# Optimization experiments

Hardware: AMD Instinct MI355X
Metric: run time of the kernel (lower is better)

Reference implementation:

```python
import jax, jax.numpy as jnp
import numpy as np

NEG_SLOPE = 0.1   # LeakyReLU slope
EPS = 1e-5        # GroupNorm eps
GROUPS = 8        # out_feat // 16 = 128 // 16
NSAMPLE = 16      # naggre (k in KNN)
FEAT = 128        # feat_dim


def leaky(x):
    return jnp.where(x >= 0, x, NEG_SLOPE * x)


def gnorm(x, gamma, beta):
    # GroupNorm over channel dim 1; works for [B,C,N] and [B,C,N,K]
    B, C = x.shape[0], x.shape[1]
    sh = x.shape
    xg = x.reshape(B, GROUPS, -1)
    m = xg.mean(-1, keepdims=True)
    v = xg.var(-1, keepdims=True)
    xg = (xg - m) * jax.lax.rsqrt(v + EPS)
    br = (1, C) + (1,) * (len(sh) - 2)
    return xg.reshape(sh) * gamma.reshape(br) + beta.reshape(br)


def conv1(x, W, b):  # 1x1 Conv1d: x [B,C,N]
    return jnp.einsum('oc,bcn->bon', W, x) + b[None, :, None]


def conv2(x, W, b):  # 1x1 Conv2d: x [B,C,N,K]
    return jnp.einsum('oc,bcnk->bonk', W, x) + b[None, :, None, None]


def knn_idx(xyz, k):
    # xyz [B,3,N] -> idx [B,N,k] of k nearest points (self included)
    pts = xyz.transpose(0, 2, 1)                      # [B,N,3]
    sq = jnp.sum(pts * pts, axis=-1)                  # [B,N]
    d2 = sq[:, :, None] + sq[:, None, :] - 2.0 * jnp.einsum('bnc,bmc->bnm', pts, pts)
    _, idx = jax.lax.top_k(-d2, k)
    return idx


# grouping_operation: feat [B,C,N], idx [B,N,K] -> [B,C,N,K]
group = jax.vmap(lambda f, i: f[:, i])


def setup_inputs() -> dict:
    key = jax.random.key(0)
    ks = jax.random.split(key, 32)
    s = 0.05
    d = {
        'xyz': jax.random.normal(ks[0], (2, 3, 8192), jnp.float32),
        'feat': jax.random.normal(ks[1], (2, FEAT, 8192), jnp.float32),
        'W_pre': jax.random.normal(ks[2], (FEAT, FEAT), jnp.float32) * s,
        'b_pre': jnp.zeros((FEAT,), jnp.float32),
        'W_pos1': jax.random.normal(ks[3], (FEAT, 3), jnp.float32) * s,
        'b_pos1': jnp.zeros((FEAT,), jnp.float32),
        'g_pos1': jnp.ones((FEAT,), jnp.float32),
        'be_pos1': jnp.zeros((FEAT,), jnp.float32),
        'W_pos2': jax.random.normal(ks[4], (FEAT, FEAT), jnp.float32) * s,
        'b_pos2': jnp.zeros((FEAT,), jnp.float32),
        'W_q': jax.random.normal(ks[5], (FEAT, FEAT), jnp.float32) * s,
        'b_q': jnp.zeros((FEAT,), jnp.float32),
        'W_k': jax.random.normal(ks[6], (FEAT, FEAT), jnp.float32) * s,
        'b_k': jnp.zeros((FEAT,), jnp.float32),
        'W_v': jax.random.normal(ks[7], (FEAT, FEAT), jnp.float32) * s,
        'b_v': jnp.zeros((FEAT,), jnp.float32),
        'W_att1': jax.random.normal(ks[8], (FEAT, FEAT), jnp.float32) * s,
        'b_att1': jnp.zeros((FEAT,), jnp.float32),
        'g_att1': jnp.ones((FEAT,), jnp.float32),
        'be_att1': jnp.zeros((FEAT,), jnp.float32),
        'W_att2': jax.random.normal(ks[9], (FEAT, FEAT), jnp.float32) * s,
        'b_att2': jnp.zeros((FEAT,), jnp.float32),
        'W_post': jax.random.normal(ks[10], (FEAT, FEAT), jnp.float32) * s,
        'b_post': jnp.zeros((FEAT,), jnp.float32),
        'g_post': jnp.ones((FEAT,), jnp.float32),
        'be_post': jnp.zeros((FEAT,), jnp.float32),
    }
    return d


def reference(xyz, feat, W_pre, b_pre, W_pos1, b_pos1, g_pos1, be_pos1,
              W_pos2, b_pos2, W_q, b_q, W_k, b_k, W_v, b_v,
              W_att1, b_att1, g_att1, be_att1, W_att2, b_att2,
              W_post, b_post, g_post, be_post):
    idx = knn_idx(xyz, NSAMPLE)                       # [B,N,K]
    new_feat = conv1(feat, W_pre, b_pre)              # [B,C,N]
    rel = group(xyz, idx) - xyz[:, :, :, None]        # [B,3,N,K]
    pos = conv2(rel, W_pos1, b_pos1)
    pos = leaky(gnorm(pos, g_pos1, be_pos1))
    pos = conv2(pos, W_pos2, b_pos2)                  # [B,C,N,K]
    q = conv1(new_feat, W_q, b_q)
    k = group(conv1(new_feat, W_k, b_k), idx)
    v = group(conv1(new_feat, W_v, b_v), idx)
    att = q[:, :, :, None] - k + pos
    att = conv2(att, W_att1, b_att1)
    att = leaky(gnorm(att, g_att1, be_att1))
    att = conv2(att, W_att2, b_att2)
    att = jax.nn.softmax(att, axis=3)                 # softmax over neighbors
    out = jnp.sum(att * v, axis=3) + new_feat         # [B,C,N]
    out = leaky(gnorm(conv1(out, W_post, b_post), g_post, be_post))
    return out
```

## Files before the change

kernel.cpp:

```cpp
#include <hip/hip_runtime.h>
#include <hip/hip_bf16.h>
#include <float.h>

#define B_ 2
#define N_ 8192
#define C_ 128
#define K_ 16
#define G_ 8
#define NK_ (N_*K_)
#define BN_ (B_*N_)
#define BNK_ (B_*NK_)
#define CN_ (C_*N_)
#define NEG 0.1f
#define EPSV 1e-5f

#define GR_ 24
#define NC_ (GR_*GR_*GR_)
#define GLOF -6.0f
#define GHF 0.5f
#define KNN_MARGIN 2e-4f
#define EMPTY_KEY 0x7FEFFFFFFFFFFFFFull

typedef __attribute__((ext_vector_type(4))) float f32x4;
typedef __attribute__((ext_vector_type(8))) short s16x8;
typedef __attribute__((ext_vector_type(4))) short s16x4;

__device__ __forceinline__ float leakyf(float x){ return x >= 0.f ? x : NEG*x; }
__device__ __forceinline__ short f2b(float x){
  union { __hip_bfloat16 b; short s; } u; u.b = __float2bfloat16(x); return u.s;
}
__device__ __forceinline__ float b2f(short s){
  union { __hip_bfloat16 b; short s; } u; u.s = s; return __bfloat162float(u.b);
}

__device__ __forceinline__ int dpp_shr1_i(int x){
  return __builtin_amdgcn_update_dpp(x, x, 0x111, 0xF, 0xF, false);
}
__device__ __forceinline__ unsigned long long dpp_shr1_u64(unsigned long long x){
  union { unsigned long long q; int i[2]; } u; u.q = x;
  u.i[0] = dpp_shr1_i(u.i[0]);
  u.i[1] = dpp_shr1_i(u.i[1]);
  return u.q;
}
__device__ __forceinline__ unsigned long long readlane_u64(unsigned long long x, int l){
  union { unsigned long long q; int i[2]; } u; u.q = x;
  union { unsigned long long q; int i[2]; } r;
  r.i[0] = __builtin_amdgcn_readlane(u.i[0], l);
  r.i[1] = __builtin_amdgcn_readlane(u.i[1], l);
  return r.q;
}
__device__ __forceinline__ unsigned long long d2key(double d2, int idx){
  d2 = fmax(d2, 0.0);
  union { double d; unsigned long long q; } u; u.d = d2;
  return (u.q & ~0x1FFFull) | (unsigned long long)idx;
}
__device__ __forceinline__ double key_upper_d2(unsigned long long k){
  union { unsigned long long q; double d; } u; u.q = k | 0x1FFFull;
  return u.d;
}
__device__ __forceinline__ int cell1(float x){
  int c = (int)floorf((x - GLOF)*(1.0f/GHF));
  return min(max(c, 0), GR_-1);
}

template<int CTRL>
__device__ __forceinline__ float dppf(float x){
  union { float f; int i; } u; u.f = x;
  u.i = __builtin_amdgcn_update_dpp(0, u.i, CTRL, 0xF, 0xF, true);
  return u.f;
}
__device__ __forceinline__ float red16(float x){
  x += dppf<0xB1>(x);
  x += dppf<0x4E>(x);
  x += dppf<0x141>(x);
  x += dppf<0x140>(x);
  return x;
}

__global__ __launch_bounds__(256) void pack_featb_kernel(const float* __restrict__ xyz,
    const float* __restrict__ feat, float4* __restrict__ pt4, ushort* __restrict__ fb,
    int* __restrict__ cellCnt){
  int e = blockIdx.x*256 + threadIdx.x;
  int b = e >> 13, n = e & (N_-1);
  const float* xb = xyz + b*3*N_;
  float x = xb[n], y = xb[N_+n], z = xb[2*N_+n];
  pt4[e] = make_float4(x, y, z, x*x + y*y + z*z);
  atomicAdd(&cellCnt[b*NC_ + (cell1(z)*GR_ + cell1(y))*GR_ + cell1(x)], 1);
  const float* xin = feat + b*CN_ + n;
  #pragma unroll
  for (int c0 = 0; c0 < C_; c0 += 8){
    s16x8 o8;
    #pragma unroll
    for (int i = 0; i < 8; i++) o8[i] = f2b(xin[(size_t)(c0+i)*N_]);
    *(s16x8*)(fb + (size_t)e*C_ + c0) = o8;
  }
}

__global__ __launch_bounds__(1024) void scan_kernel(const int* __restrict__ cnt,
    int* __restrict__ cellStart, int* __restrict__ cellCur){
  __shared__ int bs[1024];
  int t = threadIdx.x;
  int base = t*27;
  int s = 0;
  for (int i = 0; i < 27; i++) s += cnt[base+i];
  bs[t] = s;
  __syncthreads();
  for (int off = 1; off < 1024; off <<= 1){
    int v = (t >= off) ? bs[t-off] : 0;
    __syncthreads();
    bs[t] += v;
    __syncthreads();
  }
  int run = (t == 0) ? 0 : bs[t-1];
  for (int i = 0; i < 27; i++){
    cellStart[base+i] = run;
    cellCur[base+i]  = run;
    run += cnt[base+i];
  }
  if (t == 1023) cellStart[2*NC_] = BN_;
}

__global__ __launch_bounds__(256) void scatter_kernel(const float4* __restrict__ pt4,
    int* __restrict__ cellCur, float4* __restrict__ spts, int* __restrict__ sidx){
  int e = blockIdx.x*256 + threadIdx.x;
  int b = e >> 13;
  float4 p = pt4[e];
  int cid = b*NC_ + (cell1(p.z)*GR_ + cell1(p.y))*GR_ + cell1(p.x);
  int slot = atomicAdd(&cellCur[cid], 1);
  spts[slot] = p;
  sidx[slot] = e & (N_-1);
}

__global__ __launch_bounds__(512) void knn_kernel(const float4* __restrict__ pt4,
    const float4* __restrict__ spts, const int* __restrict__ sidx,
    const int* __restrict__ cellStart, int* __restrict__ idxo){
  int lane = threadIdx.x & 63, wid = threadIdx.x >> 6;
  int qg = blockIdx.x*8 + wid;
  int b = qg >> 13;
  float4 qp = spts[qg];
  int nq = sidx[qg];
  double qx = qp.x, qy = qp.y, qz = qp.z;
  double qsq = qx*qx + qy*qy + qz*qz;
  float qx2 = -2.f*qp.x, qy2 = -2.f*qp.y, qz2 = -2.f*qp.z;
  unsigned long long mykey = EMPTY_KEY;
  float cmpv = FLT_MAX;
  int ci = cell1(qp.x), cj = cell1(qp.y), ck = cell1(qp.z);

  auto process = [&](unsigned long long m, unsigned long long keyv){
    while (m){
      int src = __ffsll(m) - 1; m &= m - 1;
      unsigned long long kn = readlane_u64(keyv, src);
      bool less = kn < mykey;
      unsigned long long bm = __ballot(less) & 0xFFFFull;
      if (bm){
        int pos = __ffsll(bm) - 1;
        unsigned long long pk = dpp_shr1_u64(mykey);
        if (lane < 16){
          if (lane > pos) mykey = pk;
          else if (lane == pos) mykey = kn;
        }
      }
    }
  };

  auto do_range = [&](int cid0, int cid1){
    int s = cellStart[cid0], e = cellStart[cid1+1];
    for (int off = s; off < e; off += 64){
      int t = off + lane;
      bool valid = t < e;
      float4 pp = make_float4(0.f, 0.f, 0.f, 3.0e38f);
      int oi = 0;
      if (valid){ pp = spts[t]; oi = sidx[t]; }
      float f = fmaf(pp.x, qx2, fmaf(pp.y, qy2, fmaf(pp.z, qz2, pp.w)));
      unsigned long long m = __ballot(valid && (f < cmpv));
      if (m){
        double px = pp.x, py = pp.y, pz = pp.z;
        double psq = px*px + py*py + pz*pz;
        double dot = qx*px + qy*py + qz*pz;
        process(m, d2key(qsq + psq - 2.0*dot, oi));
        cmpv = fminf(cmpv, (float)(key_upper_d2(readlane_u64(mykey, 15)) - qsq) + KNN_MARGIN);
      }
    }
  };

  int x0 = max(ci-1, 0), x1 = min(ci+1, GR_-1);
  int cbase = b*NC_;
  do_range(cbase + (ck*GR_ + cj)*GR_ + x0, cbase + (ck*GR_ + cj)*GR_ + x1);
  for (int dz = -1; dz <= 1; dz++){
    int z = ck + dz; if (z < 0 || z >= GR_) continue;
    for (int dy = -1; dy <= 1; dy++){
      int y = cj + dy; if (y < 0 || y >= GR_) continue;
      if ((dy | dz) == 0) continue;
      do_range(cbase + (z*GR_ + y)*GR_ + x0, cbase + (z*GR_ + y)*GR_ + x1);
    }
  }

  double thr_up = key_upper_d2(readlane_u64(mykey, 15));
  if (thr_up > (double)GHF*(double)GHF){
    mykey = EMPTY_KEY;
    const float4* pts = pt4 + (b << 13);
    for (int t0 = 0; t0 < N_; t0 += 64){
      float4 pp = pts[t0 + lane];
      float f = fmaf(pp.x, qx2, fmaf(pp.y, qy2, fmaf(pp.z, qz2, pp.w)));
      unsigned long long m = __ballot(f < cmpv);
      if (m){
        double px = pp.x, py = pp.y, pz = pp.z;
        double psq = px*px + py*py + pz*pz;
        double dot = qx*px + qy*py + qz*pz;
        process(m, d2key(qsq + psq - 2.0*dot, t0 + lane));
        cmpv = fminf(cmpv, (float)(key_upper_d2(readlane_u64(mykey, 15)) - qsq) + KNN_MARGIN);
      }
    }
  }
  if (lane < 16) idxo[((size_t)(b<<13) + nq)*K_ + lane] = (int)(mykey & 0x1FFFull);
}

__global__ __launch_bounds__(256) void setup_kernel(const float* __restrict__ W_att1,
    const float* __restrict__ W_pos2, const float* __restrict__ W_q, const float* __restrict__ W_k,
    const float* __restrict__ b_pos2, const float* __restrict__ b_att1,
    const float* __restrict__ b_q, const float* __restrict__ b_k,
    float* __restrict__ Wf, float* __restrict__ Wqa, float* __restrict__ Wka,
    float* __restrict__ bG1, float* __restrict__ bqa, float* __restrict__ bka){
  int bx = blockIdx.x;
  if (bx < 192){
    int which = bx >> 6;
    const float* Bm = which==0 ? W_pos2 : (which==1 ? W_q : W_k);
    float* Cm = which==0 ? Wf : (which==1 ? Wqa : Wka);
    int e = (bx & 63)*256 + threadIdx.x;
    int o = e >> 7, c = e & 127;
    float s = 0.f;
    #pragma unroll 8
    for (int m = 0; m < 128; m++) s += W_att1[o*128+m]*Bm[m*128+c];
    Cm[e] = s;
  } else {
    for (int t = threadIdx.x; t < 384; t += 256){
      int which = t >> 7, o = t & 127;
      const float* v = which==0 ? b_pos2 : (which==1 ? b_q : b_k);
      float* out = which==0 ? bG1 : (which==1 ? bqa : bka);
      float s = which==0 ? b_att1[o] : 0.f;
      for (int m = 0; m < 128; m++) s += W_att1[o*128+m]*v[m];
      out[o] = s;
    }
  }
}

__global__ __launch_bounds__(256) void posmom_kernel(const float4* __restrict__ pt4,
    const int* __restrict__ idx, float* __restrict__ mom){
  __shared__ float ls[9];
  if (threadIdx.x < 9) ls[threadIdx.x] = 0.f;
  __syncthreads();
  int p = blockIdx.x*256 + threadIdx.x;
  int b = p >> 17;
  int n = p >> 4;
  int j = idx[p];
  float4 pj = pt4[(b<<13) + j], pn = pt4[n];
  float rx = pj.x - pn.x, ry = pj.y - pn.y, rz = pj.z - pn.z;
  float m9[9] = { rx, ry, rz, rx*rx, ry*ry, rz*rz, rx*ry, rx*rz, ry*rz };
  #pragma unroll
  for (int i = 0; i < 9; i++){
    float s = m9[i];
    #pragma unroll
    for (int mk = 32; mk; mk >>= 1) s += __shfl_xor(s, mk, 64);
    if ((threadIdx.x & 63) == 0) atomicAdd(&ls[i], s);
  }
  __syncthreads();
  if (threadIdx.x < 9) atomicAdd(&mom[b*9 + threadIdx.x], ls[threadIdx.x]);
}

__global__ void posfin_kernel(const float* __restrict__ mom,
    const float* __restrict__ W1, const float* __restrict__ b1,
    const float* __restrict__ g1, const float* __restrict__ be1, float* __restrict__ prm){
  int i = threadIdx.x;
  int b = i >> 7, c = i & 127;
  const float* M = mom + b*9;
  float wx = W1[3*c], wy = W1[3*c+1], wz = W1[3*c+2], bb = b1[c];
  const float cnt = (float)NK_;
  float wr = wx*M[0] + wy*M[1] + wz*M[2];
  float s_c = wr + bb*cnt;
  float q_c = wx*wx*M[3] + wy*wy*M[4] + wz*wz*M[5]
            + 2.f*(wx*wy*M[6] + wx*wz*M[7] + wy*wz*M[8])
            + 2.f*bb*wr + bb*bb*cnt;
  #pragma unroll
  for (int mk = 1; mk < 16; mk <<= 1){
    s_c += __shfl_xor(s_c, mk, 64);
    q_c += __shfl_xor(q_c, mk, 64);
  }
  const float invcnt = 1.0f/(16.0f*(float)NK_);
  float m = s_c*invcnt;
  float var = q_c*invcnt - m*m;
  var = fmaxf(var, 0.f);
  float r = rsqrtf(var + EPSV);
  float rs = r*g1[c];
  float4* p4 = (float4*)prm;
  p4[b*128 + c] = make_float4(wx*rs, wy*rs, wz*rs, (bb-m)*rs + be1[c]);
}

__global__ void attfin_kernel(const float* __restrict__ gsum, const float* __restrict__ gssq,
    const float* __restrict__ ga, const float* __restrict__ bea, float* __restrict__ prm, float invcnt){
  __shared__ float sm[16], sr[16];
  int i = threadIdx.x;
  if (i < 16){
    float m = gsum[i]*invcnt;
    float v = gssq[i]*invcnt - m*m;
    v = fmaxf(v, 0.f);
    sm[i] = m; sr[i] = rsqrtf(v + EPSV);
  }
  __syncthreads();
  int b = i >> 7, c = i & 127, g = c >> 4;
  float sc = ga[c]*sr[b*G_+g];
  float2* p2 = (float2*)prm;
  p2[b*128 + c] = make_float2(sc, bea[c] - sm[b*G_+g]*sc);
}

#define ST_COPY 0
#define ST_GN   1
#define ST_POS  2
#define EP_PM    0
#define EP_QKS   1
#define EP_F32CM 2

template<int STAGE>
__device__ __forceinline__ void stage_x(ushort* xs,
    const ushort* __restrict__ Xb, const float* __restrict__ prm,
    const float4* __restrict__ pt4, const int* __restrict__ idx, int p0, int b)
{
  int tid = threadIdx.x;
  int row = tid & 63, cc = tid >> 6;
  if constexpr (STAGE == ST_COPY){
    const ushort* src = Xb + (size_t)(p0+row)*C_ + cc*32;
    #pragma unroll
    for (int q = 0; q < 4; q++){
      s16x8 v8 = *(const s16x8*)(src + q*8);
      int sl = (cc*4+q) ^ (row&7);
      *(s16x8*)(xs + row*C_ + sl*8) = v8;
    }
  } else if constexpr (STAGE == ST_GN){
    const ushort* src = Xb + (size_t)(p0+row)*C_ + cc*32;
    const float2* pr = (const float2*)prm + b*128;
    #pragma unroll
    for (int q = 0; q < 4; q++){
      s16x8 v8 = *(const s16x8*)(src + q*8);
      s16x8 o8;
      #pragma unroll
      for (int i = 0; i < 8; i++){
        int c = cc*32 + q*8 + i;
        float2 s2 = pr[c];
        o8[i] = f2b(leakyf(b2f(v8[i])*s2.x + s2.y));
      }
      int sl = (cc*4+q) ^ (row&7);
      *(s16x8*)(xs + row*C_ + sl*8) = o8;
    }
  } else {
    int p = p0 + row;
    int ng = p >> 4;
    int j = idx[p];
    float4 pj = pt4[(b<<13) + j], pn = pt4[ng];
    float rx = pj.x - pn.x, ry = pj.y - pn.y, rz = pj.z - pn.z;
    const float4* pr = (const float4*)prm + b*128;
    #pragma unroll
    for (int q = 0; q < 4; q++){
      s16x8 o8;
      #pragma unroll
      for (int i = 0; i < 8; i++){
        int c = cc*32 + q*8 + i;
        float4 s4 = pr[c];
        o8[i] = f2b(leakyf(fmaf(s4.x, rx, fmaf(s4.y, ry, fmaf(s4.z, rz, s4.w)))));
      }
      int sl = (cc*4+q) ^ (row&7);
      *(s16x8*)(xs + row*C_ + sl*8) = o8;
    }
  }
}

__device__ __forceinline__ void load_afr(s16x8 afr[2][4], const float* __restrict__ W, int wid, int lm, int lh){
  #pragma unroll
  for (int t = 0; t < 2; t++){
    int T = wid*2 + t;
    #pragma unroll
    for (int ks = 0; ks < 4; ks++){
      const float* wr = W + (size_t)(T*16 + lm)*C_ + ks*32 + lh*8;
      float4 w0 = *(const float4*)wr;
      float4 w1 = *(const float4*)(wr+4);
      s16x8 a;
      a[0]=f2b(w0.x); a[1]=f2b(w0.y); a[2]=f2b(w0.z); a[3]=f2b(w0.w);
      a[4]=f2b(w1.x); a[5]=f2b(w1.y); a[6]=f2b(w1.z); a[7]=f2b(w1.w);
      afr[t][ks] = a;
    }
  }
}

__device__ __forceinline__ void mfma_tile(f32x4 acc[2][4], const s16x8 afr[2][4],
    const ushort* xs, const float* __restrict__ bias, int wid, int lm, int lh)
{
  #pragma unroll
  for (int t = 0; t < 2; t++){
    f32x4 bs = *(const f32x4*)(bias + (wid*2+t)*16 + lh*4);
    #pragma unroll
    for (int ps = 0; ps < 4; ps++) acc[t][ps] = bs;
  }
  #pragma unroll
  for (int ps = 0; ps < 4; ps++){
    int row = ps*16 + lm;
    s16x8 bf[4];
    #pragma unroll
    for (int ks = 0; ks < 4; ks++){
      int sl = (ks*4+lh) ^ (row&7);
      bf[ks] = *(const s16x8*)(xs + row*C_ + sl*8);
    }
    #pragma unroll
    for (int ks = 0; ks < 4; ks++){
      #pragma unroll
      for (int t = 0; t < 2; t++)
        acc[t][ps] = __builtin_amdgcn_mfma_f32_16x16x32_bf16(afr[t][ks], bf[ks], acc[t][ps], 0,0,0);
    }
  }
}

template<int STAGE, int EPI>
__device__ __forceinline__ void mgemm_body(ushort* xs, float* sblk,
    const ushort* __restrict__ Xb, const float* __restrict__ W, const float* __restrict__ bias,
    const float* __restrict__ prm, const float4* __restrict__ pt4, const int* __restrict__ idx,
    const ushort* __restrict__ Aq, const ushort* __restrict__ Ak,
    void* __restrict__ Y, float* __restrict__ gsum, float* __restrict__ gssq, int bsh, int bx)
{
  int tid = threadIdx.x;
  int l = tid & 63, wid = tid >> 6;
  int lm = l & 15, lh = l >> 4;
  int p0 = bx * 64;
  int b = p0 >> bsh;

  if (tid < 16) sblk[tid] = 0.f;

  s16x8 afr[2][4];
  load_afr(afr, W, wid, lm, lh);
  stage_x<STAGE>(xs, Xb, prm, pt4, idx, p0, b);
  __syncthreads();

  f32x4 acc[2][4];
  mfma_tile(acc, afr, xs, bias, wid, lm, lh);

  float gs[2] = {0.f,0.f}, gq[2] = {0.f,0.f};
  #pragma unroll
  for (int t = 0; t < 2; t++){
    int T = wid*2 + t;
    int o0 = T*16 + lh*4;
    #pragma unroll
    for (int ps = 0; ps < 4; ps++){
      int p = p0 + ps*16 + lm;
      if constexpr (EPI == EP_PM){
        s16x4 r4;
        #pragma unroll
        for (int r = 0; r < 4; r++) r4[r] = f2b(acc[t][ps][r]);
        *(s16x4*)((ushort*)Y + (size_t)p*C_ + o0) = r4;
      } else if constexpr (EPI == EP_QKS){
        int ng = p >> 4;
        int j = idx[p];
        s16x4 aq4 = *(const s16x4*)(Aq + (size_t)ng*C_ + o0);
        s16x4 ak4 = *(const s16x4*)(Ak + ((size_t)(b<<13)+j)*C_ + o0);
        s16x4 r4;
        #pragma unroll
        for (int r = 0; r < 4; r++){
          float v = acc[t][ps][r] + b2f(aq4[r]) - b2f(ak4[r]);
          r4[r] = f2b(v);
          gs[t] += v; gq[t] += v*v;
        }
        *(s16x4*)((ushort*)Y + (size_t)p*C_ + o0) = r4;
      } else {
        float* yf = (float*)Y;
        #pragma unroll
        for (int r = 0; r < 4; r++){
          float v = acc[t][ps][r];
          yf[(size_t)(o0+r)*BN_ + p] = v;
          gs[t] += v; gq[t] += v*v;
        }
      }
    }
  }

  if constexpr (EPI == EP_QKS || EPI == EP_F32CM){
    #pragma unroll
    for (int t = 0; t < 2; t++){
      float s = gs[t], q = gq[t];
      #pragma unroll
      for (int mk = 32; mk; mk >>= 1){ s += __shfl_xor(s, mk, 64); q += __shfl_xor(q, mk, 64); }
      if (l == 0){
        int T = wid*2 + t;
        atomicAdd(&sblk[T], s); atomicAdd(&sblk[8+T], q);
      }
    }
    __syncthreads();
    if (tid < 8){
      atomicAdd(&gsum[b*G_ + tid], sblk[tid]);
      atomicAdd(&gssq[b*G_ + tid], sblk[8+tid]);
    }
  }
}

template<int STAGE, int EPI>
__global__ __launch_bounds__(256) void mgemm_kernel(
    const ushort* __restrict__ Xb, const float* __restrict__ W, const float* __restrict__ bias,
    const float* __restrict__ prm, const float4* __restrict__ pt4, const int* __restrict__ idx,
    const ushort* __restrict__ Aq, const ushort* __restrict__ Ak,
    void* __restrict__ Y, float* __restrict__ gsum, float* __restrict__ gssq, int bsh)
{
  __shared__ ushort xs[64*128];
  __shared__ float sblk[16];
  mgemm_body<STAGE,EPI>(xs, sblk, Xb, W, bias, prm, pt4, idx, Aq, Ak, Y, gsum, gssq, bsh, blockIdx.x);
}

__global__ __launch_bounds__(256) void qkv_kernel(const ushort* __restrict__ nfb,
    const float* __restrict__ Wv, const float* __restrict__ bv,
    const float* __restrict__ Wqa, const float* __restrict__ bqa,
    const float* __restrict__ Wka, const float* __restrict__ bka,
    ushort* __restrict__ vb, ushort* __restrict__ Aqb, ushort* __restrict__ Akb)
{
  __shared__ ushort xs[64*128];
  __shared__ float sblk[16];
  if (blockIdx.y == 0)
    mgemm_body<ST_COPY,EP_PM>(xs, sblk, nfb, Wv, bv, nullptr, nullptr, nullptr, nullptr, nullptr, vb, nullptr, nullptr, 13, blockIdx.x);
  else if (blockIdx.y == 1)
    mgemm_body<ST_COPY,EP_PM>(xs, sblk, nfb, Wqa, bqa, nullptr, nullptr, nullptr, nullptr, nullptr, Aqb, nullptr, nullptr, 13, blockIdx.x);
  else
    mgemm_body<ST_COPY,EP_PM>(xs, sblk, nfb, Wka, bka, nullptr, nullptr, nullptr, nullptr, nullptr, Akb, nullptr, nullptr, 13, blockIdx.x);
}

__global__ __launch_bounds__(256) void fatt_kernel(const ushort* __restrict__ Xb ,
    const float* __restrict__ W , const float* __restrict__ bias ,
    const float* __restrict__ prm , const int* __restrict__ idx,
    const ushort* __restrict__ vb, const ushort* __restrict__ nfb, ushort* __restrict__ outb)
{
  __shared__ ushort xs[64*128];
  int tid = threadIdx.x;
  int l = tid & 63, wid = tid >> 6;
  int lm = l & 15, lh = l >> 4;
  int p0 = blockIdx.x * 64;
  int b = p0 >> 17;

  s16x4 vpre[2][4];
  #pragma unroll
  for (int ps = 0; ps < 4; ps++){
    int p = p0 + ps*16 + lm;
    int j = idx[p];
    const ushort* vr = vb + ((size_t)(b<<13)+j)*C_ + lh*4;
    #pragma unroll
    for (int t = 0; t < 2; t++)
      vpre[t][ps] = *(const s16x4*)(vr + (wid*2+t)*16);
  }

  s16x8 afr[2][4];
  load_afr(afr, W, wid, lm, lh);
  stage_x<ST_GN>(xs, Xb, prm, nullptr, nullptr, p0, b);
  __syncthreads();

  f32x4 acc[2][4];
  mfma_tile(acc, afr, xs, bias, wid, lm, lh);

  #pragma unroll
  for (int t = 0; t < 2; t++){
    int o0 = (wid*2+t)*16 + lh*4;
    #pragma unroll
    for (int ps = 0; ps < 4; ps++){
      s16x4 v4 = vpre[t][ps];
      f32x4 e, pv;
      #pragma unroll
      for (int r = 0; r < 4; r++){
        float ev = __expf(acc[t][ps][r]);
        e[r] = ev;
        pv[r] = ev * b2f(v4[r]);
      }
      #pragma unroll
      for (int r = 0; r < 4; r++){
        e[r]  = red16(e[r]);
        pv[r] = red16(pv[r]);
      }
      if (lm == 0){
        int n = (p0 + ps*16) >> 4;
        s16x4 n4 = *(const s16x4*)(nfb + (size_t)n*C_ + o0);
        s16x4 o4;
        #pragma unroll
        for (int r = 0; r < 4; r++) o4[r] = f2b(pv[r]/e[r] + b2f(n4[r]));
        *(s16x4*)(outb + (size_t)n*C_ + o0) = o4;
      }
    }
  }
}

__global__ __launch_bounds__(256) void final_kernel(const float* __restrict__ out1,
    const float* __restrict__ gsum, const float* __restrict__ gssq,
    const float* __restrict__ g, const float* __restrict__ be, float* __restrict__ out){
  int e = blockIdx.x*256 + threadIdx.x;
  int b = e >> 20;
  int c = (e >> 13) & (C_-1);
  int n = e & (N_-1);
  int gi = b*G_ + (c >> 4);
  const float invcnt = 1.0f/(float)(16*N_);
  float m = gsum[gi]*invcnt;
  float var = gssq[gi]*invcnt - m*m;
  var = fmaxf(var, 0.f);
  float r = rsqrtf(var + EPSV);
  float v = (out1[(size_t)c*BN_ + b*N_ + n] - m) * r;
  v = v*g[c] + be[c];
  out[e] = leakyf(v);
}

extern "C" void kernel_launch(void* const* d_in, const int* in_sizes, int n_in,
                              void* d_out, int out_size, void* d_ws, size_t ws_size,
                              hipStream_t stream) {
  const float* xyz    = (const float*)d_in[0];
  const float* feat   = (const float*)d_in[1];
  const float* W_pre  = (const float*)d_in[2];
  const float* b_pre  = (const float*)d_in[3];
  const float* W_pos1 = (const float*)d_in[4];
  const float* b_pos1 = (const float*)d_in[5];
  const float* g_pos1 = (const float*)d_in[6];
  const float* be_pos1= (const float*)d_in[7];
  const float* W_pos2 = (const float*)d_in[8];
  const float* b_pos2 = (const float*)d_in[9];
  const float* W_q    = (const float*)d_in[10];
  const float* b_q    = (const float*)d_in[11];
  const float* W_k    = (const float*)d_in[12];
  const float* b_k    = (const float*)d_in[13];
  const float* W_v    = (const float*)d_in[14];
  const float* b_v    = (const float*)d_in[15];
  const float* W_att1 = (const float*)d_in[16];
  const float* b_att1 = (const float*)d_in[17];
  const float* g_att1 = (const float*)d_in[18];
  const float* be_att1= (const float*)d_in[19];
  const float* W_att2 = (const float*)d_in[20];
  const float* b_att2 = (const float*)d_in[21];
  const float* W_post = (const float*)d_in[22];
  const float* b_post = (const float*)d_in[23];
  const float* g_post = (const float*)d_in[24];
  const float* be_post= (const float*)d_in[25];

  char* w = (char*)d_ws;
  float4* pt4 = (float4*)w;            w += sizeof(float4)*BN_;
  int* idx = (int*)w;                  w += sizeof(int)*BNK_;
  ushort* fb   = (ushort*)w;           w += (size_t)2*BN_*C_;
  ushort* nfb  = (ushort*)w;           w += (size_t)2*BN_*C_;
  ushort* vb   = (ushort*)w;           w += (size_t)2*BN_*C_;
  ushort* Aqb  = (ushort*)w;           w += (size_t)2*BN_*C_;
  ushort* Akb  = (ushort*)w;           w += (size_t)2*BN_*C_;
  ushort* outb = (ushort*)w;           w += (size_t)2*BN_*C_;
  float* out1  = (float*)w;            w += (size_t)4*BN_*C_;
  ushort* bufA = (ushort*)w;           w += (size_t)2*BNK_*C_;
  float* Wf    = (float*)w;            w += sizeof(float)*C_*C_;
  float* Wqa   = (float*)w;            w += sizeof(float)*C_*C_;
  float* Wka   = (float*)w;            w += sizeof(float)*C_*C_;
  float* bG1   = (float*)w;            w += 512;
  float* bqa   = (float*)w;            w += 512;
  float* bka   = (float*)w;            w += 512;
  float* posPrm= (float*)w;            w += sizeof(float)*1024;
  float* attPrm= (float*)w;            w += sizeof(float)*512;
  float* stats = (float*)w;            w += 1024;
  int* cellCnt = (int*)w;              w += sizeof(int)*2*NC_;
  int* cellStart=(int*)w;              w += sizeof(int)*(2*NC_+1);
  int* cellCur = (int*)w;              w += sizeof(int)*2*NC_;
  float4* spts = (float4*)w;           w += sizeof(float4)*BN_;
  int* sidx    = (int*)w;              w += sizeof(int)*BN_;

  float* posMom = stats + 0;
  float* att_sum = stats + 64, *att_ssq = stats + 80;
  float* post_sum= stats +128, *post_ssq= stats +144;

  hipMemsetAsync(stats, 0, 1024, stream);
  hipMemsetAsync(cellCnt, 0, sizeof(int)*2*NC_, stream);

  pack_featb_kernel<<<BN_/256, 256, 0, stream>>>(xyz, feat, pt4, fb, cellCnt);
  scan_kernel<<<1, 1024, 0, stream>>>(cellCnt, cellStart, cellCur);
  scatter_kernel<<<BN_/256, 256, 0, stream>>>(pt4, cellCur, spts, sidx);
  knn_kernel<<<BN_/8, 512, 0, stream>>>(pt4, spts, sidx, cellStart, idx);

  setup_kernel<<<193, 256, 0, stream>>>(W_att1, W_pos2, W_q, W_k, b_pos2, b_att1, b_q, b_k,
      Wf, Wqa, Wka, bG1, bqa, bka);

  mgemm_kernel<ST_COPY,EP_PM><<<BN_/64, 256, 0, stream>>>(fb, W_pre, b_pre, nullptr, nullptr, nullptr,
      nullptr, nullptr, nfb, nullptr, nullptr, 13);
  qkv_kernel<<<dim3(BN_/64, 3), 256, 0, stream>>>(nfb, W_v, b_v, Wqa, bqa, Wka, bka, vb, Aqb, Akb);

  posmom_kernel<<<BNK_/256, 256, 0, stream>>>(pt4, idx, posMom);
  posfin_kernel<<<1, 256, 0, stream>>>(posMom, W_pos1, b_pos1, g_pos1, be_pos1, posPrm);

  mgemm_kernel<ST_POS,EP_QKS><<<BNK_/64, 256, 0, stream>>>(nullptr, Wf, bG1, posPrm, pt4, idx,
      Aqb, Akb, bufA, att_sum, att_ssq, 17);
  attfin_kernel<<<1, 256, 0, stream>>>(att_sum, att_ssq, g_att1, be_att1, attPrm, 1.0f/(float)(16.0*NK_));

  fatt_kernel<<<BNK_/64, 256, 0, stream>>>(bufA, W_att2, b_att2, attPrm, idx, vb, nfb, outb);

  mgemm_kernel<ST_COPY,EP_F32CM><<<BN_/64, 256, 0, stream>>>(outb, W_post, b_post, nullptr, nullptr, nullptr,
      nullptr, nullptr, out1, post_sum, post_ssq, 13);
  final_kernel<<<(B_*CN_)/256, 256, 0, stream>>>(out1, post_sum, post_ssq, g_post, be_post, (float*)d_out);
}
```

Before: 337.4 us.

## Double-buffer fatt tiles across two sub-tiles and unroll KNN brute-force scan

The fused attention kernel now processes two 64-row tiles per block. It uses double-buffered shared memory and prefetches the second tile's activations and gathered V rows into registers while the first tile's MFMA and epilogue run. This amortises the weight-fragment load and hides global-load latency, at the cost of more registers and LDS per block and half as many blocks. Separately, the KNN brute-force fallback loop is unrolled to test two 64-point chunks per iteration, which increases memory-level parallelism.

```diff
diff --git a/kernel.cpp b/kernel.cpp
--- a/kernel.cpp
+++ b/kernel.cpp
@@ -199,15 +199,26 @@
   if (thr_up > (double)GHF*(double)GHF){
     mykey = EMPTY_KEY;
     const float4* pts = pt4 + (b << 13);
-    for (int t0 = 0; t0 < N_; t0 += 64){
-      float4 pp = pts[t0 + lane];
-      float f = fmaf(pp.x, qx2, fmaf(pp.y, qy2, fmaf(pp.z, qz2, pp.w)));
-      unsigned long long m = __ballot(f < cmpv);
-      if (m){
-        double px = pp.x, py = pp.y, pz = pp.z;
-        double psq = px*px + py*py + pz*pz;
-        double dot = qx*px + qy*py + qz*pz;
-        process(m, d2key(qsq + psq - 2.0*dot, t0 + lane));
+    for (int t0 = 0; t0 < N_; t0 += 128){
+      float4 pA = pts[t0 + lane];
+      float4 pB = pts[t0 + 64 + lane];
+      float fA = fmaf(pA.x, qx2, fmaf(pA.y, qy2, fmaf(pA.z, qz2, pA.w)));
+      float fB = fmaf(pB.x, qx2, fmaf(pB.y, qy2, fmaf(pB.z, qz2, pB.w)));
+      unsigned long long mA = __ballot(fA < cmpv);
+      unsigned long long mB = __ballot(fB < cmpv);
+      if (mA | mB){
+        if (mA){
+          double px = pA.x, py = pA.y, pz = pA.z;
+          double psq = px*px + py*py + pz*pz;
+          double dot = qx*px + qy*py + qz*pz;
+          process(mA, d2key(qsq + psq - 2.0*dot, t0 + lane));
+        }
+        if (mB){
+          double px = pB.x, py = pB.y, pz = pB.z;
+          double psq = px*px + py*py + pz*pz;
+          double dot = qx*px + qy*py + qz*pz;
+          process(mB, d2key(qsq + psq - 2.0*dot, t0 + 64 + lane));
+        }
         cmpv = fminf(cmpv, (float)(key_upper_d2(readlane_u64(mykey, 15)) - qsq) + KNN_MARGIN);
       }
     }
@@ -529,60 +540,98 @@
     const float* __restrict__ prm , const int* __restrict__ idx,
     const ushort* __restrict__ vb, const ushort* __restrict__ nfb, ushort* __restrict__ outb)
 {
-  __shared__ ushort xs[64*128];
+  __shared__ ushort xs[2][64*C_];
   int tid = threadIdx.x;
   int l = tid & 63, wid = tid >> 6;
   int lm = l & 15, lh = l >> 4;
-  int p0 = blockIdx.x * 64;
-  int b = p0 >> 17;
-
-  s16x4 vpre[2][4];
-  #pragma unroll
-  for (int ps = 0; ps < 4; ps++){
-    int p = p0 + ps*16 + lm;
-    int j = idx[p];
-    const ushort* vr = vb + ((size_t)(b<<13)+j)*C_ + lh*4;
-    #pragma unroll
-    for (int t = 0; t < 2; t++)
-      vpre[t][ps] = *(const s16x4*)(vr + (wid*2+t)*16);
-  }
+  int row = tid & 63, cc = tid >> 6;
+  int base = blockIdx.x * 128;
+  int b = base >> 17;
+  const float2* pr = (const float2*)prm + b*128;
+
+  auto load_tile = [&](int p0, s16x8 L[4]){
+    const ushort* src = Xb + (size_t)(p0+row)*C_ + cc*32;
+    #pragma unroll
+    for (int q = 0; q < 4; q++) L[q] = *(const s16x8*)(src + q*8);
+  };
+  auto load_vpre = [&](int p0, s16x4 vp[2][4]){
+    #pragma unroll
+    for (int ps = 0; ps < 4; ps++){
+      int p = p0 + ps*16 + lm;
+      int j = idx[p];
+      const ushort* vr = vb + ((size_t)(b<<13)+j)*C_ + lh*4;
+      #pragma unroll
+      for (int t = 0; t < 2; t++) vp[t][ps] = *(const s16x4*)(vr + (wid*2+t)*16);
+    }
+  };
+  auto commit_tile = [&](const s16x8 L[4], ushort* dst){
+    #pragma unroll
+    for (int q = 0; q < 4; q++){
+      s16x8 o8;
+      #pragma unroll
+      for (int i = 0; i < 8; i++){
+        int c = cc*32 + q*8 + i;
+        float2 s2 = pr[c];
+        o8[i] = f2b(leakyf(b2f(L[q][i])*s2.x + s2.y));
+      }
+      int sl = (cc*4+q) ^ (row&7);
+      *(s16x8*)(dst + row*C_ + sl*8) = o8;
+    }
+  };
+  auto epilogue = [&](int p0, f32x4 acc[2][4], const s16x4 vp[2][4]){
+    #pragma unroll
+    for (int t = 0; t < 2; t++){
+      int o0 = (wid*2+t)*16 + lh*4;
+      #pragma unroll
+      for (int ps = 0; ps < 4; ps++){
+        s16x4 v4 = vp[t][ps];
+        f32x4 e, pv;
+        #pragma unroll
+        for (int r = 0; r < 4; r++){
+          float ev = __expf(acc[t][ps][r]);
+          e[r] = ev;
+          pv[r] = ev * b2f(v4[r]);
+        }
+        #pragma unroll
+        for (int r = 0; r < 4; r++){
+          e[r]  = red16(e[r]);
+          pv[r] = red16(pv[r]);
+        }
+        if (lm == 0){
+          int n = (p0 + ps*16) >> 4;
+          s16x4 n4 = *(const s16x4*)(nfb + (size_t)n*C_ + o0);
+          s16x4 o4;
+          #pragma unroll
+          for (int r = 0; r < 4; r++) o4[r] = f2b(pv[r]/e[r] + b2f(n4[r]));
+          *(s16x4*)(outb + (size_t)n*C_ + o0) = o4;
+        }
+      }
+    }
+  };
 
   s16x8 afr[2][4];
   load_afr(afr, W, wid, lm, lh);
-  stage_x<ST_GN>(xs, Xb, prm, nullptr, nullptr, p0, b);
+
+  s16x8 L0[4];
+  s16x4 vp0[2][4];
+  load_tile(base, L0);
+  load_vpre(base, vp0);
+  commit_tile(L0, xs[0]);
+  s16x8 L1[4];
+  s16x4 vp1[2][4];
+  load_tile(base + 64, L1);
+  load_vpre(base + 64, vp1);
   __syncthreads();
 
   f32x4 acc[2][4];
-  mfma_tile(acc, afr, xs, bias, wid, lm, lh);
-
-  #pragma unroll
-  for (int t = 0; t < 2; t++){
-    int o0 = (wid*2+t)*16 + lh*4;
-    #pragma unroll
-    for (int ps = 0; ps < 4; ps++){
-      s16x4 v4 = vpre[t][ps];
-      f32x4 e, pv;
-      #pragma unroll
-      for (int r = 0; r < 4; r++){
-        float ev = __expf(acc[t][ps][r]);
-        e[r] = ev;
-        pv[r] = ev * b2f(v4[r]);
-      }
-      #pragma unroll
-      for (int r = 0; r < 4; r++){
-        e[r]  = red16(e[r]);
-        pv[r] = red16(pv[r]);
-      }
-      if (lm == 0){
-        int n = (p0 + ps*16) >> 4;
-        s16x4 n4 = *(const s16x4*)(nfb + (size_t)n*C_ + o0);
-        s16x4 o4;
-        #pragma unroll
-        for (int r = 0; r < 4; r++) o4[r] = f2b(pv[r]/e[r] + b2f(n4[r]));
-        *(s16x4*)(outb + (size_t)n*C_ + o0) = o4;
-      }
-    }
-  }
+  mfma_tile(acc, afr, xs[0], bias, wid, lm, lh);
+  epilogue(base, acc, vp0);
+
+  commit_tile(L1, xs[1]);
+  __syncthreads();
+
+  mfma_tile(acc, afr, xs[1], bias, wid, lm, lh);
+  epilogue(base + 64, acc, vp1);
 }
 
 __global__ __launch_bounds__(256) void final_kernel(const float* __restrict__ out1,
@@ -685,7 +734,7 @@
       Aqb, Akb, bufA, att_sum, att_ssq, 17);
   attfin_kernel<<<1, 256, 0, stream>>>(att_sum, att_ssq, g_att1, be_att1, attPrm, 1.0f/(float)(16.0*NK_));
 
-  fatt_kernel<<<BNK_/64, 256, 0, stream>>>(bufA, W_att2, b_att2, attPrm, idx, vb, nfb, outb);
+  fatt_kernel<<<BNK_/128, 256, 0, stream>>>(bufA, W_att2, b_att2, attPrm, idx, vb, nfb, outb);
 
   mgemm_kernel<ST_COPY,EP_F32CM><<<BN_/64, 256, 0, stream>>>(outb, W_post, b_post, nullptr, nullptr, nullptr,
       nullptr, nullptr, out1, post_sum, post_ssq, 13);
```

New measurement: 335.8 us. About the same (-0.5%).
